# Performance work log

Hardware: AMD Instinct MI355X
Metric: run time of the kernel (lower is better)

Reference implementation:

```python
import jax, jax.numpy as jnp
import numpy as np
import math

B, L, D = 4, 4096, 1024
PI = math.pi
LN_EPS = 1e-5


def setup_inputs() -> dict:
    key = jax.random.key(0)
    ks = jax.random.split(key, 16)
    s = 1.0 / math.sqrt(D)
    inp = {
        "x": jax.random.normal(ks[0], (B, L, D), dtype=jnp.float32),
        # Linear weights stored as [in, out] (torch W.T)
        "Wk": jax.random.normal(ks[1], (D, D), dtype=jnp.float32) * s,
        "bk": jnp.zeros((D,), dtype=jnp.float32),
        "Wq": jax.random.normal(ks[2], (D, D), dtype=jnp.float32) * s,
        "bq": jnp.zeros((D,), dtype=jnp.float32),
        "Wv": jax.random.normal(ks[3], (D, D), dtype=jnp.float32) * s,
        "bv": jnp.zeros((D,), dtype=jnp.float32),
        "ln_g": jnp.ones((D,), dtype=jnp.float32),
        "ln_b": jnp.zeros((D,), dtype=jnp.float32),
        "Wo": jax.random.normal(ks[4], (D, D), dtype=jnp.float32) * s,
        "bo": jnp.zeros((D,), dtype=jnp.float32),
        "Wg1": jax.random.normal(ks[5], (D, D // 4), dtype=jnp.float32) * s,
        "bg1": jnp.zeros((D // 4,), dtype=jnp.float32),
        "Wg2": jax.random.normal(ks[6], (D // 4, 1), dtype=jnp.float32) * (2.0 / math.sqrt(D)),
        "bg2": jnp.zeros((1,), dtype=jnp.float32),
        "pos_phases": jax.random.normal(ks[7], (L, D), dtype=jnp.float32) * PI,
    }
    return inp


def _layernorm(x, g, b):
    mu = jnp.mean(x, axis=-1, keepdims=True)
    var = jnp.var(x, axis=-1, keepdims=True)
    return (x - mu) * jax.lax.rsqrt(var + LN_EPS) * g + b


def reference(x, Wk, bk, Wq, bq, Wv, bv, ln_g, ln_b, Wo, bo, Wg1, bg1, Wg2, bg2, pos_phases):
    # dropout is identity in eval mode
    key_phases = jnp.tanh(x @ Wk + bk) * PI          # [B,L,D]
    query_phases = jnp.tanh(x @ Wq + bq) * PI        # [B,L,D]
    V = x @ Wv + bv                                   # [B,L,D]

    cos_k, sin_k = jnp.cos(key_phases), jnp.sin(key_phases)
    cos_q, sin_q = jnp.cos(query_phases), jnp.sin(query_phases)

    mem_real = jnp.cumsum(V * cos_k, axis=1)
    mem_imag = jnp.cumsum(V * sin_k, axis=1)
    content_retrieved = mem_real * cos_q + mem_imag * sin_q

    pp = pos_phases[: x.shape[1]]                     # [L,D]
    cos_p, sin_p = jnp.cos(pp), jnp.sin(pp)
    pos_mem_real = jnp.cumsum(V * cos_p, axis=1)
    pos_mem_imag = jnp.cumsum(V * sin_p, axis=1)
    pos_retrieved = pos_mem_real * cos_p + pos_mem_imag * sin_p

    gate = jax.nn.sigmoid(jax.nn.gelu(x @ Wg1 + bg1) @ Wg2 + bg2)  # [B,L,1]
    combined = gate * content_retrieved + (1.0 - gate) * pos_retrieved

    positions = jnp.arange(1, x.shape[1] + 1, dtype=jnp.float32)
    norm = jnp.sqrt(positions)[None, :, None]
    out = _layernorm(combined / norm, ln_g, ln_b) @ Wo + bo
    return x + out
```

## Files before the change

kernel.cpp:

```cpp
#include <hip/hip_runtime.h>
#include <math.h>

#define B_ 4
#define L_ 4096
#define D_ 1024
#define DG_ 256
#define NC_ 256
#define CL_ 16
#define PI_F 3.14159265358979323846f
#define LN_EPS_F 1e-5f

typedef __attribute__((ext_vector_type(8))) _Float16 f16x8;
typedef __attribute__((ext_vector_type(8))) short s16x8;
typedef __attribute__((ext_vector_type(4))) short s16x4;
typedef __attribute__((ext_vector_type(4))) float f32x4;

__device__ inline short f2h(float f) { return __builtin_bit_cast(short, (_Float16)f); }
__device__ inline float h2f(short s) { return (float)__builtin_bit_cast(_Float16, s); }

__device__ inline float ftanh(float x) {
    float e = __expf(2.0f * x);
    return 1.0f - 2.0f / (e + 1.0f);
}
__device__ inline void fsincos(float x, float* s, float* c) {
    *s = __sinf(x); *c = __cosf(x);
}

__device__ inline void gld16(const void* g, void* l) {
    __builtin_amdgcn_global_load_lds(
        (const __attribute__((address_space(1))) unsigned int*)g,
        (__attribute__((address_space(3))) unsigned int*)l, 16, 0, 0);
}

__global__ __launch_bounds__(256)
void conv_x(const float* __restrict__ x, short* __restrict__ xh, int n8)
{
    int t = blockIdx.x * 256 + threadIdx.x;
    if (t >= n8) return;
    const float4* p = (const float4*)x + (size_t)t * 2;
    float4 a = p[0], b = p[1];
    s16x8 v;
    v[0] = f2h(a.x); v[1] = f2h(a.y); v[2] = f2h(a.z); v[3] = f2h(a.w);
    v[4] = f2h(b.x); v[5] = f2h(b.y); v[6] = f2h(b.z); v[7] = f2h(b.w);
    *(s16x8*)(xh + (size_t)t * 8) = v;
}

__global__ __launch_bounds__(256)
void convT(const float* __restrict__ W, short* __restrict__ Th, int N)
{
    __shared__ float tile[64][65];
    const int n0 = blockIdx.x * 64, k0 = blockIdx.y * 64;
    const int t = threadIdx.x;
    const int r = t >> 4, c4 = (t & 15) * 4;

    #pragma unroll
    for (int i = 0; i < 4; ++i) {
        float4 v = *(const float4*)&W[(size_t)(k0 + r + i * 16) * N + n0 + c4];
        tile[r + i * 16][c4 + 0] = v.x;
        tile[r + i * 16][c4 + 1] = v.y;
        tile[r + i * 16][c4 + 2] = v.z;
        tile[r + i * 16][c4 + 3] = v.w;
    }
    __syncthreads();
    #pragma unroll
    for (int i = 0; i < 4; ++i) {
        const int n = r + i * 16;
        s16x4 o;
        o[0] = f2h(tile[c4 + 0][n]);
        o[1] = f2h(tile[c4 + 1][n]);
        o[2] = f2h(tile[c4 + 2][n]);
        o[3] = f2h(tile[c4 + 3][n]);
        *(s16x4*)&Th[(size_t)(n0 + n) * 1024 + k0 + c4] = o;
    }
}

#define BARRIER() __builtin_amdgcn_s_barrier()
#define PRIO1() __builtin_amdgcn_s_setprio(1)
#define PRIO0() __builtin_amdgcn_s_setprio(0)
#define LGKM0() do { asm volatile("s_waitcnt lgkmcnt(0)" ::: "memory"); \
                     __builtin_amdgcn_sched_barrier(0); } while (0)
#define VMC(N) asm volatile("s_waitcnt vmcnt(" #N ")" ::: "memory")

#define DSR(dst, areg, OFS)                                              \
    asm volatile("ds_read_b128 %0, %1 offset:" OFS                       \
                 : "=v"(dst) : "v"(areg))

#define RDA4(areg)                                                       \
    DSR(af[0], areg, "0");    DSR(af[1], areg, "2048");                  \
    DSR(af[2], areg, "4096"); DSR(af[3], areg, "6144");
#define RDA4H(areg)                                                      \
    DSR(af[0], areg, "8192");  DSR(af[1], areg, "10240");                \
    DSR(af[2], areg, "12288"); DSR(af[3], areg, "14336");
#define RDB4(areg, KK)                                                   \
    DSR(bq[0][KK], areg, "0");    DSR(bq[1][KK], areg, "2048");          \
    DSR(bq[2][KK], areg, "4096"); DSR(bq[3][KK], areg, "6144");

#define MF(MG, KK)                                                       \
    _Pragma("unroll") for (int i_ = 0; i_ < 4; ++i_)                     \
    _Pragma("unroll") for (int n_ = 0; n_ < 4; ++n_)                     \
        acc[(MG)*4 + i_][n_] = __builtin_amdgcn_mfma_f32_16x16x32_f16(   \
            af[i_], bq[n_][KK], acc[(MG)*4 + i_][n_], 0, 0, 0);

template<int EPI, typename OT>
__global__ __launch_bounds__(512, 2)
void mgemm256(const short* __restrict__ A, const short* __restrict__ Bt,
              const float* __restrict__ X, OT* __restrict__ out0,
              short* __restrict__ out1, short* __restrict__ out2,
              const float* __restrict__ b0, const float* __restrict__ b1,
              const float* __restrict__ b2, int M, int N, int K)
{
    extern __shared__ char lds[];

    const int tid = threadIdx.x;
    const int w = tid >> 6, l = tid & 63;
    const int wr = w >> 2, wc = w & 3;
    const int fr = l & 15, kb = l >> 4;
    const int bm = blockIdx.x * 256, bn = blockIdx.y * 256;
    const int np = K >> 7;

    const int s = fr & 7;
    const int cK0 = (((s >> 2) & 1) << 6) | (((kb ^ s) & 3) << 4);
    const int aA0 = (wr << 14) + fr * 128 + cK0;
    const int aA1 = aA0 ^ 64;
    const int aB0 = 32768 + ((wc >> 1) << 14) + ((wc & 1) * 64 + fr) * 128 + cK0;
    const int aB1 = aB0 ^ 64;
    const int aA0o = aA0 + 65536, aA1o = aA1 + 65536;
    const int aB0o = aB0 + 65536, aB1o = aB1 + 65536;

    const int p0 = tid * 16;
    const int sr = p0 >> 7;
    const int sc = (p0 & 127) ^ ((sr & 7) << 4);
    const short* gA = A  + (size_t)(bm + sr) * K + (sc >> 1);
    const short* gB = Bt + (size_t)(bn + sr) * K + (sc >> 1);
    char* ldst = lds + (w << 10);
    const size_t q1 = (size_t)64 * K, q2 = 2 * q1, q3 = 3 * q1;

    f32x4 acc[8][4] = {};
    f16x8 af[4];
    f16x8 bq[4][2];

    gld16(gA,      ldst);          gld16(gA + q1, ldst + 8192);
    gld16(gA + q2, ldst + 16384);  gld16(gA + q3, ldst + 24576);
    gld16(gB,      ldst + 32768);  gld16(gB + q1, ldst + 40960);
    gld16(gB + q2, ldst + 49152);  gld16(gB + q3, ldst + 57344);
    gld16(gA +      64, ldst + 65536);
    gld16(gA + q2 + 64, ldst + 65536 + 16384);
    VMC(2);
    BARRIER();

    const short* gAn = gA + 64;
    const short* gBn = gB + 64;

    for (int pp = 0; pp < np; ++pp) {
        const bool nl = (pp + 1 < np);

        RDA4(aA0); RDB4(aB0, 0);
        gld16(gBn,      ldst + 98304);
        gld16(gBn + q1, ldst + 98304 + 8192);
        LGKM0();
        PRIO1(); MF(0, 0); PRIO0();
        RDA4(aA1); RDB4(aB1, 1);
        gld16(gBn + q2, ldst + 98304 + 16384);
        gld16(gBn + q3, ldst + 98304 + 24576);
        LGKM0();
        PRIO1(); MF(0, 1); PRIO0();
        BARRIER();
        RDA4H(aA0);
        gld16(gAn + q1, ldst + 65536 + 8192);
        gld16(gAn + q3, ldst + 65536 + 24576);
        LGKM0();
        PRIO1(); MF(1, 0); PRIO0();
        RDA4H(aA1);
        if (nl) { gld16(gAn + 64, ldst); gld16(gAn + 64 + q2, ldst + 16384); }
        LGKM0();
        PRIO1(); MF(1, 1); PRIO0();
        if (nl) { VMC(2); } else { VMC(0); }
        BARRIER();

        RDA4(aA0o); RDB4(aB0o, 0);
        if (nl) {
            gld16(gBn +      64, ldst + 32768);
            gld16(gBn + q1 + 64, ldst + 40960);
        }
        LGKM0();
        PRIO1(); MF(0, 0); PRIO0();
        RDA4(aA1o); RDB4(aB1o, 1);
        if (nl) {
            gld16(gBn + q2 + 64, ldst + 49152);
            gld16(gBn + q3 + 64, ldst + 57344);
        }
        LGKM0();
        PRIO1(); MF(0, 1); PRIO0();
        BARRIER();
        RDA4H(aA0o);
        if (nl) {
            gld16(gAn + q1 + 64, ldst + 8192);
            gld16(gAn + q3 + 64, ldst + 24576);
        }
        LGKM0();
        PRIO1(); MF(1, 0); PRIO0();
        RDA4H(aA1o);
        if (nl) { gld16(gAn + 128, ldst + 65536); gld16(gAn + 128 + q2, ldst + 65536 + 16384); }
        LGKM0();
        PRIO1(); MF(1, 1); PRIO0();
        if (nl) {
            VMC(2);
            BARRIER();
        }
        gAn += 128; gBn += 128;
    }

    if constexpr (EPI == 4) {
        short* op; const float* bp; bool dt;
        if (bn < 1024)      { op = (short*)out0; bp = b0; dt = true;  }
        else if (bn < 2048) { op = out1;         bp = b1; dt = true;  }
        else                { op = out2;         bp = b2; dt = false; }
        const int cb = bn & 1023;
        float bc[4];
        #pragma unroll
        for (int nf = 0; nf < 4; ++nf) bc[nf] = bp[cb + wc * 64 + nf * 16 + fr];
        #pragma unroll
        for (int mf = 0; mf < 8; ++mf)
            #pragma unroll
            for (int rr = 0; rr < 4; ++rr) {
                const int row = bm + wr * 128 + mf * 16 + kb * 4 + rr;
                #pragma unroll
                for (int nf = 0; nf < 4; ++nf) {
                    const int cc = cb + wc * 64 + nf * 16 + fr;
                    float c = acc[mf][nf][rr] + bc[nf];
                    if (dt) c = ftanh(c) * PI_F;
                    op[(size_t)row * 1024 + cc] = f2h(c);
                }
            }
    } else {
        float bc[4];
        #pragma unroll
        for (int nf = 0; nf < 4; ++nf) bc[nf] = b0[bn + wc * 64 + nf * 16 + fr];
        #pragma unroll
        for (int mf = 0; mf < 8; ++mf)
            #pragma unroll
            for (int rr = 0; rr < 4; ++rr) {
                const int row = bm + wr * 128 + mf * 16 + kb * 4 + rr;
                #pragma unroll
                for (int nf = 0; nf < 4; ++nf) {
                    const int col = bn + wc * 64 + nf * 16 + fr;
                    float c = acc[mf][nf][rr] + bc[nf] + X[(size_t)row * N + col];
                    ((float*)out0)[(size_t)row * N + col] = c;
                }
            }
    }
}

#define RDAF(areg)                                                       \
    DSR(af[0], areg, "0");    DSR(af[1], areg, "2048");                  \
    DSR(af[2], areg, "4096"); DSR(af[3], areg, "6144");
#define RDBF(areg)                                                       \
    DSR(bqs[0], areg, "0");    DSR(bqs[1], areg, "2048");                \
    DSR(bqs[2], areg, "4096"); DSR(bqs[3], areg, "6144");

#define MF16()                                                           \
    _Pragma("unroll") for (int i_ = 0; i_ < 4; ++i_)                     \
    _Pragma("unroll") for (int n_ = 0; n_ < 4; ++n_)                     \
        acc[i_][n_] = __builtin_amdgcn_mfma_f32_16x16x32_f16(            \
            af[i_], bqs[n_], acc[i_][n_], 0, 0, 0);

template<int EPI>
__global__ __launch_bounds__(256, 2)
void gemm128(const short* __restrict__ A, const short* __restrict__ Bt,
             const float* __restrict__ b0, const float* __restrict__ wg2p,
             float* __restrict__ gatep, int M, int N, int K)
{
    extern __shared__ char lds[];

    const int tid = threadIdx.x;
    const int w = tid >> 6, l = tid & 63;
    const int wr = w >> 1, wc = w & 1;
    const int fr = l & 15, kb = l >> 4;
    const int bm = blockIdx.x * 128, bn = blockIdx.y * 128;

    const int s = fr & 7;
    const int cK0 = (((s >> 2) & 1) << 6) | (((kb ^ s) & 3) << 4);
    const int aA0e = (wr * 64 + fr) * 128 + cK0;
    const int aA1e = aA0e ^ 64;
    const int aB0e = 16384 + (wc * 64 + fr) * 128 + cK0;
    const int aB1e = aB0e ^ 64;
    const int aA0o = aA0e + 32768, aA1o = aA1e + 32768;
    const int aB0o = aB0e + 32768, aB1o = aB1e + 32768;

    const int p16 = tid * 16;
    const int sr = p16 >> 7;
    const int sc = (p16 & 127) ^ ((sr & 7) << 4);
    const short* gA = A  + (size_t)(bm + sr) * K + (sc >> 1);
    const short* gB = Bt + (size_t)(bn + sr) * K + (sc >> 1);
    char* ldA = lds + (w << 10);
    const size_t r32 = (size_t)32 * K;

    f32x4 acc[4][4] = {};
    f16x8 af[4], bqs[4];

    #pragma unroll
    for (int i = 0; i < 4; ++i) gld16(gA + i * r32, ldA + i * 4096);
    #pragma unroll
    for (int i = 0; i < 4; ++i) gld16(gB + i * r32, ldA + 16384 + i * 4096);
    VMC(0);
    BARRIER();

    const short* gAt = gA;
    const short* gBt = gB;
    const int np = K >> 7;

    for (int pp = 0; pp < np; ++pp) {
        const bool nl = (pp + 1 < np);

        RDAF(aA0e); RDBF(aB0e);
        #pragma unroll
        for (int i = 0; i < 4; ++i) gld16(gAt + 64 + i * r32, ldA + 32768 + i * 4096);
        LGKM0();
        PRIO1(); MF16(); PRIO0();
        RDAF(aA1e); RDBF(aB1e);
        #pragma unroll
        for (int i = 0; i < 4; ++i) gld16(gBt + 64 + i * r32, ldA + 49152 + i * 4096);
        LGKM0();
        PRIO1(); MF16(); PRIO0();
        VMC(0);
        BARRIER();

        RDAF(aA0o); RDBF(aB0o);
        if (nl) {
            #pragma unroll
            for (int i = 0; i < 4; ++i) gld16(gAt + 128 + i * r32, ldA + i * 4096);
        }
        LGKM0();
        PRIO1(); MF16(); PRIO0();
        RDAF(aA1o); RDBF(aB1o);
        if (nl) {
            #pragma unroll
            for (int i = 0; i < 4; ++i) gld16(gBt + 128 + i * r32, ldA + 16384 + i * 4096);
        }
        LGKM0();
        PRIO1(); MF16(); PRIO0();
        if (nl) {
            VMC(0);
            BARRIER();
        }
        gAt += 128; gBt += 128;
    }

    float bg[4], wg[4];
    #pragma unroll
    for (int nf = 0; nf < 4; ++nf) {
        const int cl = bn + wc * 64 + nf * 16 + fr;
        bg[nf] = b0[cl];
        wg[nf] = wg2p[cl];
    }
    #pragma unroll
    for (int mf = 0; mf < 4; ++mf)
        #pragma unroll
        for (int rr = 0; rr < 4; ++rr) {
            const int row = bm + wr * 64 + mf * 16 + kb * 4 + rr;
            float part = 0.f;
            #pragma unroll
            for (int nf = 0; nf < 4; ++nf) {
                float c = acc[mf][nf][rr] + bg[nf];
                float tt = 0.7978845608028654f * (c + 0.044715f * c * c * c);
                float g = 0.5f * c * (1.0f + ftanh(tt));
                part += g * wg[nf];
            }
            part += __shfl_xor(part, 1);
            part += __shfl_xor(part, 2);
            part += __shfl_xor(part, 4);
            part += __shfl_xor(part, 8);
            if (fr == 0) atomicAdd(&gatep[row], part);
        }
}

__global__ __launch_bounds__(256)
void passA(const short* __restrict__ V, const short* __restrict__ KP,
           const float* __restrict__ PP, f32x4* __restrict__ SI)
{
    const int bid = blockIdx.x;
    const int b = bid >> 8, c = bid & 255;
    const int d0 = threadIdx.x * 4;

    f32x4 cr = {}, ci = {}, pr = {}, pi = {};
    const size_t base  = ((size_t)b * L_ + (size_t)c * CL_) * D_ + d0;
    const size_t pbase = (size_t)c * CL_ * D_ + d0;
    for (int ll = 0; ll < CL_; ++ll) {
        s16x4 v4  = *(const s16x4*)&V [base + (size_t)ll * D_];
        s16x4 kp4 = *(const s16x4*)&KP[base + (size_t)ll * D_];
        f32x4 pp4 = *(const f32x4*)&PP[pbase + (size_t)ll * D_];
        #pragma unroll
        for (int j = 0; j < 4; ++j) {
            float v = h2f(v4[j]);
            float sk, ck, sp, cp;
            fsincos(h2f(kp4[j]), &sk, &ck);
            fsincos(pp4[j], &sp, &cp);
            cr[j] += v * ck; ci[j] += v * sk;
            pr[j] += v * cp; pi[j] += v * sp;
        }
    }
    const size_t sidx = ((size_t)bid << 10) + d0;
    #pragma unroll
    for (int j = 0; j < 4; ++j) {
        f32x4 o = { cr[j], ci[j], pr[j], pi[j] };
        SI[sidx + j] = o;
    }
}

__global__ __launch_bounds__(256)
void passB(f32x4* __restrict__ SI)
{
    const int t = blockIdx.x * 256 + threadIdx.x;
    const int b = t >> 10, d = t & 1023;
    f32x4 run = {};
    for (int c = 0; c < NC_; ++c) {
        const size_t idx = ((size_t)(b * NC_ + c) << 10) + d;
        f32x4 v = SI[idx];
        SI[idx] = run;
        run += v;
    }
}

__global__ __launch_bounds__(256)
void passC(const short* __restrict__ V, const short* KP,
           const short* __restrict__ QP, const float* __restrict__ PP,
           const float* __restrict__ gatep, const float* __restrict__ bg2,
           const f32x4* __restrict__ SI, const float* __restrict__ ln_g,
           const float* __restrict__ ln_b, short* Yb)
{
    const int bid = blockIdx.x;
    const int b = bid >> 8, c = bid & 255;
    const int d0 = threadIdx.x * 4;

    const size_t sidx = ((size_t)bid << 10) + d0;
    f32x4 cr, ci, pr, pi;
    #pragma unroll
    for (int j = 0; j < 4; ++j) {
        f32x4 s0 = SI[sidx + j];
        cr[j] = s0[0]; ci[j] = s0[1]; pr[j] = s0[2]; pi[j] = s0[3];
    }
    const f32x4 g_ln = *(const f32x4*)&ln_g[d0];
    const f32x4 b_ln = *(const f32x4*)&ln_b[d0];
    const float bg2v = bg2[0];

    __shared__ float2 lred[2][4];
    const int wid = threadIdx.x >> 6;
    const int lane = threadIdx.x & 63;

    const int lbase = c * CL_;
    size_t off = ((size_t)b * L_ + lbase) * D_ + d0;
    s16x4 v4  = *(const s16x4*)&V [off];
    s16x4 kp4 = *(const s16x4*)&KP[off];
    s16x4 qp4 = *(const s16x4*)&QP[off];
    f32x4 pp4 = *(const f32x4*)&PP[(size_t)lbase * D_ + d0];
    float gpre = gatep[b * L_ + lbase];

    for (int l0 = 0; l0 < CL_; ++l0) {
        const int ll = lbase + l0;
        const size_t offn = off + D_;
        s16x4 v4n = v4, kp4n = kp4, qp4n = qp4;
        f32x4 pp4n = pp4; float gpn = gpre;
        if (l0 + 1 < CL_) {
            v4n  = *(const s16x4*)&V [offn];
            kp4n = *(const s16x4*)&KP[offn];
            qp4n = *(const s16x4*)&QP[offn];
            pp4n = *(const f32x4*)&PP[(size_t)(ll + 1) * D_ + d0];
            gpn  = gatep[b * L_ + ll + 1];
        }

        const float gv = 1.0f / (1.0f + __expf(-(gpre + bg2v)));
        const float rs_pos = rsqrtf((float)(ll + 1));

        f32x4 u;
        #pragma unroll
        for (int j = 0; j < 4; ++j) {
            float v = h2f(v4[j]);
            float sk, ck, sq, cq, sp, cp;
            fsincos(h2f(kp4[j]), &sk, &ck);
            fsincos(h2f(qp4[j]), &sq, &cq);
            fsincos(pp4[j], &sp, &cp);
            cr[j] += v * ck; ci[j] += v * sk;
            pr[j] += v * cp; pi[j] += v * sp;
            float content = cr[j] * cq + ci[j] * sq;
            float posr    = pr[j] * cp + pi[j] * sp;
            u[j] = (gv * content + (1.0f - gv) * posr) * rs_pos;
        }

        float s  = u[0] + u[1] + u[2] + u[3];
        float s2 = u[0]*u[0] + u[1]*u[1] + u[2]*u[2] + u[3]*u[3];
        #pragma unroll
        for (int o = 32; o; o >>= 1) {
            s  += __shfl_down(s, o);
            s2 += __shfl_down(s2, o);
        }
        const int pb = l0 & 1;
        if (lane == 0) lred[pb][wid] = make_float2(s, s2);
        asm volatile("s_waitcnt lgkmcnt(0)" ::: "memory");
        __builtin_amdgcn_s_barrier();
        float ts  = lred[pb][0].x + lred[pb][1].x + lred[pb][2].x + lred[pb][3].x;
        float ts2 = lred[pb][0].y + lred[pb][1].y + lred[pb][2].y + lred[pb][3].y;
        const float mu  = ts * (1.0f / D_);
        const float var = ts2 * (1.0f / D_) - mu * mu;
        const float rsv = rsqrtf(var + LN_EPS_F);
        s16x4 yo;
        #pragma unroll
        for (int j = 0; j < 4; ++j)
            yo[j] = f2h((u[j] - mu) * rsv * g_ln[j] + b_ln[j]);
        *(s16x4*)&Yb[off] = yo;

        off = offn;
        v4 = v4n; kp4 = kp4n; qp4 = qp4n; pp4 = pp4n; gpre = gpn;
    }
}

extern "C" void kernel_launch(void* const* d_in, const int* in_sizes, int n_in,
                              void* d_out, int out_size, void* d_ws, size_t ws_size,
                              hipStream_t stream)
{
    const float* x    = (const float*)d_in[0];
    const float* Wk   = (const float*)d_in[1];
    const float* bk   = (const float*)d_in[2];
    const float* Wq   = (const float*)d_in[3];
    const float* bq   = (const float*)d_in[4];
    const float* Wv   = (const float*)d_in[5];
    const float* bv   = (const float*)d_in[6];
    const float* ln_g = (const float*)d_in[7];
    const float* ln_b = (const float*)d_in[8];
    const float* Wo   = (const float*)d_in[9];
    const float* bo   = (const float*)d_in[10];
    const float* Wg1  = (const float*)d_in[11];
    const float* bg1  = (const float*)d_in[12];
    const float* Wg2  = (const float*)d_in[13];
    const float* bg2  = (const float*)d_in[14];
    const float* PP   = (const float*)d_in[15];

    float* out = (float*)d_out;

    const size_t BLD   = (size_t)B_ * L_ * D_;
    const size_t SZ_X  = BLD * 2;
    const size_t SZ_R1 = (size_t)B_ * L_ * DG_ * 2;
    const size_t SZ_G1 = (size_t)D_ * DG_ * 2;
    const size_t SZ_GT = (size_t)B_ * L_ * 4;
    const size_t NEED  = SZ_X + SZ_R1 + SZ_G1 + 3 * SZ_X + SZ_GT;
    if (ws_size < NEED) {
        hipMemcpyAsync(d_out, d_in[0], BLD * sizeof(float),
                       hipMemcpyDeviceToDevice, stream);
        return;
    }

    char* wsb = (char*)d_ws;
    short* xh   = (short*)(wsb);
    char*  r1   = wsb + SZ_X;
    short* Wcat = (short*)r1;
    short* Wg1T = (short*)(r1 + SZ_R1);
    short* KP   = (short*)(r1 + SZ_R1 + SZ_G1);
    short* QP   = (short*)((char*)KP + SZ_X);
    short* V    = (short*)((char*)QP + SZ_X);
    float* gatep = (float*)((char*)V + SZ_X);
    short* WtO  = (short*)(wsb);
    f32x4* SI   = (f32x4*)(wsb + 2097152);
    short* Yb   = KP;

    const int M = B_ * L_;
    dim3 blk(256);

    conv_x<<<(int)(BLD / 8 / 256), blk, 0, stream>>>(x, xh, (int)(BLD / 8));
    dim3 gT(D_ / 64, 16);
    dim3 gTg(DG_ / 64, 16);
    convT<<<gT, blk, 0, stream>>>(Wk, Wcat + (size_t)0 * D_ * D_, D_);
    convT<<<gT, blk, 0, stream>>>(Wq, Wcat + (size_t)1 * D_ * D_, D_);
    convT<<<gT, blk, 0, stream>>>(Wv, Wcat + (size_t)2 * D_ * D_, D_);
    convT<<<gTg, blk, 0, stream>>>(Wg1, Wg1T, DG_);
    hipMemsetAsync(gatep, 0, SZ_GT, stream);

    dim3 gQKV(M / 256, 3072 / 256);
    hipLaunchKernelGGL((mgemm256<4, short>), gQKV, dim3(512), 131072, stream,
                       xh, Wcat, nullptr, KP, QP, V, bk, bq, bv, M, 3072, D_);
    dim3 gH(M / 128, DG_ / 128);
    hipLaunchKernelGGL((gemm128<5>), gH, blk, 65536, stream,
                       xh, Wg1T, bg1, Wg2, gatep, M, DG_, D_);

    convT<<<gT, blk, 0, stream>>>(Wo, WtO, D_);

    passA<<<B_ * NC_, blk, 0, stream>>>(V, KP, PP, SI);
    passB<<<(B_ * D_) / 256, blk, 0, stream>>>(SI);
    passC<<<B_ * NC_, blk, 0, stream>>>(V, KP, QP, PP, gatep, bg2, SI,
                                        ln_g, ln_b, Yb);

    dim3 gO(M / 256, D_ / 256);
    hipLaunchKernelGGL((mgemm256<3, float>), gO, dim3(512), 131072, stream,
                       Yb, WtO, x, out, nullptr, nullptr, bo, nullptr, nullptr,
                       M, D_, D_);
}
```

Before: 290.6 us.

## Precompute positional sincos, two-level chunk scan, reorder GEMM A-tile prefetch

Positional sin/cos is computed once into a half-precision table rather than being recomputed per batch in passA and passC. Chunks grow from 16 to 32 rows, and the serial per-column chunk scan becomes a two-level segmented scan (passB1 plus passB2), so fewer threads sit on a long serial dependency. In the GEMM main loop, the A-tile half loads are issued before the barrier instead of after it, to overlap them with more MFMA work. The costs are two extra small launches, extra workspace, and fp16 rounding of the positional sin/cos values, along with a risk that the earlier A loads overwrite LDS that is still being read.

Result: faster. 282.7 us (-2.7%).

```diff
diff --git a/kernel.cpp b/kernel.cpp
--- a/kernel.cpp
+++ b/kernel.cpp
@@ -5,8 +5,10 @@
 #define L_ 4096
 #define D_ 1024
 #define DG_ 256
-#define NC_ 256
-#define CL_ 16
+#define NC_ 128
+#define CL_ 32
+#define SEGL_ 8
+#define NSEG_ 16
 #define PI_F 3.14159265358979323846f
 #define LN_EPS_F 1e-5f
 
@@ -43,6 +45,23 @@
     v[0] = f2h(a.x); v[1] = f2h(a.y); v[2] = f2h(a.z); v[3] = f2h(a.w);
     v[4] = f2h(b.x); v[5] = f2h(b.y); v[6] = f2h(b.z); v[7] = f2h(b.w);
     *(s16x8*)(xh + (size_t)t * 8) = v;
+}
+
+__global__ __launch_bounds__(256)
+void csp_kernel(const float* __restrict__ PP, short* __restrict__ CSP, int n4)
+{
+    int t = blockIdx.x * 256 + threadIdx.x;
+    if (t >= n4) return;
+    f32x4 p = *(const f32x4*)&PP[(size_t)t * 4];
+    s16x8 o;
+    #pragma unroll
+    for (int j = 0; j < 4; ++j) {
+        float s, c;
+        fsincos(p[j], &s, &c);
+        o[2 * j] = f2h(c);
+        o[2 * j + 1] = f2h(s);
+    }
+    *(s16x8*)&CSP[(size_t)t * 8] = o;
 }
 
 __global__ __launch_bounds__(256)
@@ -162,12 +181,12 @@
         RDA4(aA1); RDB4(aB1, 1);
         gld16(gBn + q2, ldst + 98304 + 16384);
         gld16(gBn + q3, ldst + 98304 + 24576);
+        gld16(gAn + q1, ldst + 65536 + 8192);
+        gld16(gAn + q3, ldst + 65536 + 24576);
         LGKM0();
         PRIO1(); MF(0, 1); PRIO0();
         BARRIER();
         RDA4H(aA0);
-        gld16(gAn + q1, ldst + 65536 + 8192);
-        gld16(gAn + q3, ldst + 65536 + 24576);
         LGKM0();
         PRIO1(); MF(1, 0); PRIO0();
         RDA4H(aA1);
@@ -188,15 +207,13 @@
         if (nl) {
             gld16(gBn + q2 + 64, ldst + 49152);
             gld16(gBn + q3 + 64, ldst + 57344);
+            gld16(gAn + q1 + 64, ldst + 8192);
+            gld16(gAn + q3 + 64, ldst + 24576);
         }
         LGKM0();
         PRIO1(); MF(0, 1); PRIO0();
         BARRIER();
         RDA4H(aA0o);
-        if (nl) {
-            gld16(gAn + q1 + 64, ldst + 8192);
-            gld16(gAn + q3 + 64, ldst + 24576);
-        }
         LGKM0();
         PRIO1(); MF(1, 0); PRIO0();
         RDA4H(aA1o);
@@ -376,25 +393,25 @@
 
 __global__ __launch_bounds__(256)
 void passA(const short* __restrict__ V, const short* __restrict__ KP,
-           const float* __restrict__ PP, f32x4* __restrict__ SI)
+           const short* __restrict__ CSP, f32x4* __restrict__ SI)
 {
     const int bid = blockIdx.x;
-    const int b = bid >> 8, c = bid & 255;
+    const int b = bid >> 7, c = bid & 127;
     const int d0 = threadIdx.x * 4;
 
     f32x4 cr = {}, ci = {}, pr = {}, pi = {};
     const size_t base  = ((size_t)b * L_ + (size_t)c * CL_) * D_ + d0;
-    const size_t pbase = (size_t)c * CL_ * D_ + d0;
+    const size_t pcs   = ((size_t)c * CL_ * D_ + d0) * 2;
     for (int ll = 0; ll < CL_; ++ll) {
         s16x4 v4  = *(const s16x4*)&V [base + (size_t)ll * D_];
         s16x4 kp4 = *(const s16x4*)&KP[base + (size_t)ll * D_];
-        f32x4 pp4 = *(const f32x4*)&PP[pbase + (size_t)ll * D_];
+        s16x8 c8  = *(const s16x8*)&CSP[pcs + (size_t)ll * (D_ * 2)];
         #pragma unroll
         for (int j = 0; j < 4; ++j) {
             float v = h2f(v4[j]);
-            float sk, ck, sp, cp;
+            float sk, ck;
             fsincos(h2f(kp4[j]), &sk, &ck);
-            fsincos(pp4[j], &sp, &cp);
+            float cp = h2f(c8[2 * j]), sp = h2f(c8[2 * j + 1]);
             cr[j] += v * ck; ci[j] += v * sk;
             pr[j] += v * cp; pi[j] += v * sp;
         }
@@ -408,35 +425,56 @@
 }
 
 __global__ __launch_bounds__(256)
-void passB(f32x4* __restrict__ SI)
-{
-    const int t = blockIdx.x * 256 + threadIdx.x;
+void passB1(f32x4* __restrict__ SI, f32x4* __restrict__ STS)
+{
+    const int seg = blockIdx.x & (NSEG_ - 1);
+    const int t = (blockIdx.x >> 4) * 256 + threadIdx.x;
     const int b = t >> 10, d = t & 1023;
     f32x4 run = {};
-    for (int c = 0; c < NC_; ++c) {
+    #pragma unroll
+    for (int i = 0; i < SEGL_; ++i) {
+        const int c = seg * SEGL_ + i;
         const size_t idx = ((size_t)(b * NC_ + c) << 10) + d;
         f32x4 v = SI[idx];
         SI[idx] = run;
         run += v;
     }
+    STS[((size_t)(b * NSEG_ + seg) << 10) + d] = run;
+}
+
+__global__ __launch_bounds__(256)
+void passB2(f32x4* __restrict__ STS)
+{
+    const int t = blockIdx.x * 256 + threadIdx.x;
+    const int b = t >> 10, d = t & 1023;
+    f32x4 run = {};
+    #pragma unroll
+    for (int seg = 0; seg < NSEG_; ++seg) {
+        const size_t idx = ((size_t)(b * NSEG_ + seg) << 10) + d;
+        f32x4 v = STS[idx];
+        STS[idx] = run;
+        run += v;
+    }
 }
 
 __global__ __launch_bounds__(256)
 void passC(const short* __restrict__ V, const short* KP,
-           const short* __restrict__ QP, const float* __restrict__ PP,
+           const short* __restrict__ QP, const short* __restrict__ CSP,
            const float* __restrict__ gatep, const float* __restrict__ bg2,
-           const f32x4* __restrict__ SI, const float* __restrict__ ln_g,
-           const float* __restrict__ ln_b, short* Yb)
+           const f32x4* __restrict__ SI, const f32x4* __restrict__ STS,
+           const float* __restrict__ ln_g, const float* __restrict__ ln_b,
+           short* Yb)
 {
     const int bid = blockIdx.x;
-    const int b = bid >> 8, c = bid & 255;
+    const int b = bid >> 7, c = bid & 127;
     const int d0 = threadIdx.x * 4;
 
     const size_t sidx = ((size_t)bid << 10) + d0;
+    const size_t tidx = ((size_t)(b * NSEG_ + (c >> 3)) << 10) + d0;
     f32x4 cr, ci, pr, pi;
     #pragma unroll
     for (int j = 0; j < 4; ++j) {
-        f32x4 s0 = SI[sidx + j];
+        f32x4 s0 = SI[sidx + j] + STS[tidx + j];
         cr[j] = s0[0]; ci[j] = s0[1]; pr[j] = s0[2]; pi[j] = s0[3];
     }
     const f32x4 g_ln = *(const f32x4*)&ln_g[d0];
@@ -449,22 +487,23 @@
 
     const int lbase = c * CL_;
     size_t off = ((size_t)b * L_ + lbase) * D_ + d0;
+    size_t cso = ((size_t)lbase * D_ + d0) * 2;
     s16x4 v4  = *(const s16x4*)&V [off];
     s16x4 kp4 = *(const s16x4*)&KP[off];
     s16x4 qp4 = *(const s16x4*)&QP[off];
-    f32x4 pp4 = *(const f32x4*)&PP[(size_t)lbase * D_ + d0];
+    s16x8 c8  = *(const s16x8*)&CSP[cso];
     float gpre = gatep[b * L_ + lbase];
 
     for (int l0 = 0; l0 < CL_; ++l0) {
         const int ll = lbase + l0;
         const size_t offn = off + D_;
         s16x4 v4n = v4, kp4n = kp4, qp4n = qp4;
-        f32x4 pp4n = pp4; float gpn = gpre;
+        s16x8 c8n = c8; float gpn = gpre;
         if (l0 + 1 < CL_) {
             v4n  = *(const s16x4*)&V [offn];
             kp4n = *(const s16x4*)&KP[offn];
             qp4n = *(const s16x4*)&QP[offn];
-            pp4n = *(const f32x4*)&PP[(size_t)(ll + 1) * D_ + d0];
+            c8n  = *(const s16x8*)&CSP[cso + D_ * 2];
             gpn  = gatep[b * L_ + ll + 1];
         }
 
@@ -475,10 +514,10 @@
         #pragma unroll
         for (int j = 0; j < 4; ++j) {
             float v = h2f(v4[j]);
-            float sk, ck, sq, cq, sp, cp;
+            float sk, ck, sq, cq;
             fsincos(h2f(kp4[j]), &sk, &ck);
             fsincos(h2f(qp4[j]), &sq, &cq);
-            fsincos(pp4[j], &sp, &cp);
+            float cp = h2f(c8[2 * j]), sp = h2f(c8[2 * j + 1]);
             cr[j] += v * ck; ci[j] += v * sk;
             pr[j] += v * cp; pi[j] += v * sp;
             float content = cr[j] * cq + ci[j] * sq;
@@ -486,15 +525,15 @@
             u[j] = (gv * content + (1.0f - gv) * posr) * rs_pos;
         }
 
-        float s  = u[0] + u[1] + u[2] + u[3];
+        float sm  = u[0] + u[1] + u[2] + u[3];
         float s2 = u[0]*u[0] + u[1]*u[1] + u[2]*u[2] + u[3]*u[3];
         #pragma unroll
         for (int o = 32; o; o >>= 1) {
-            s  += __shfl_down(s, o);
+            sm += __shfl_down(sm, o);
             s2 += __shfl_down(s2, o);
         }
         const int pb = l0 & 1;
-        if (lane == 0) lred[pb][wid] = make_float2(s, s2);
+        if (lane == 0) lred[pb][wid] = make_float2(sm, s2);
         asm volatile("s_waitcnt lgkmcnt(0)" ::: "memory");
         __builtin_amdgcn_s_barrier();
         float ts  = lred[pb][0].x + lred[pb][1].x + lred[pb][2].x + lred[pb][3].x;
@@ -508,8 +547,8 @@
             yo[j] = f2h((u[j] - mu) * rsv * g_ln[j] + b_ln[j]);
         *(s16x4*)&Yb[off] = yo;
 
-        off = offn;
-        v4 = v4n; kp4 = kp4n; qp4 = qp4n; pp4 = pp4n; gpre = gpn;
+        off = offn; cso += D_ * 2;
+        v4 = v4n; kp4 = kp4n; qp4 = qp4n; c8 = c8n; gpre = gpn;
     }
 }
 
@@ -559,6 +598,8 @@
     float* gatep = (float*)((char*)V + SZ_X);
     short* WtO  = (short*)(wsb);
     f32x4* SI   = (f32x4*)(wsb + 2097152);
+    short* CSP  = (short*)(wsb + 2097152 + 8388608);
+    f32x4* STS  = (f32x4*)(wsb + 2097152 + 8388608 + 16777216);
     short* Yb   = KP;
 
     const int M = B_ * L_;
@@ -581,10 +622,13 @@
                        xh, Wg1T, bg1, Wg2, gatep, M, DG_, D_);
 
     convT<<<gT, blk, 0, stream>>>(Wo, WtO, D_);
-
-    passA<<<B_ * NC_, blk, 0, stream>>>(V, KP, PP, SI);
-    passB<<<(B_ * D_) / 256, blk, 0, stream>>>(SI);
-    passC<<<B_ * NC_, blk, 0, stream>>>(V, KP, QP, PP, gatep, bg2, SI,
+    csp_kernel<<<(int)((size_t)L_ * D_ / 4 / 256), blk, 0, stream>>>(
+        PP, CSP, (int)((size_t)L_ * D_ / 4));
+
+    passA<<<B_ * NC_, blk, 0, stream>>>(V, KP, CSP, SI);
+    passB1<<<(B_ * D_ / 256) * NSEG_, blk, 0, stream>>>(SI, STS);
+    passB2<<<B_ * D_ / 256, blk, 0, stream>>>(STS);
+    passC<<<B_ * NC_, blk, 0, stream>>>(V, KP, QP, CSP, gatep, bg2, SI, STS,
                                         ln_g, ln_b, Yb);
 
     dim3 gO(M / 256, D_ / 256);
```
